# Kernel tuning notes

Measured on AMD Instinct MI355X. Metric: run time of the kernel, lower is better.

Reference implementation:

```python
import jax, jax.numpy as jnp
import numpy as np

D = 1024
H = 16
HD = D // H
N_TEXT = 256
N_VISION = 256
N_FRAMES = 12


def setup_inputs() -> dict:
    key = jax.random.key(0)
    ks = jax.random.split(key, 10)
    s = 1.0 / np.sqrt(D)
    return {
        "text_hidden_states": jax.random.normal(ks[0], (N_TEXT, D), jnp.float32),
        "vision_hidden_states": jax.random.normal(ks[1], (N_VISION, N_FRAMES, D), jnp.float32),
        "wq": jax.random.normal(ks[2], (D, D), jnp.float32) * s,
        "bq": jnp.zeros((D,), jnp.float32),
        "wk": jax.random.normal(ks[3], (D, D), jnp.float32) * s,
        "bk": jnp.zeros((D,), jnp.float32),
        "wv": jax.random.normal(ks[4], (D, D), jnp.float32) * s,
        "bv": jnp.zeros((D,), jnp.float32),
        "wo": jax.random.normal(ks[5], (D, D), jnp.float32) * s,
        "bo": jnp.zeros((D,), jnp.float32),
    }


def reference(text_hidden_states, vision_hidden_states, wq, bq, wk, bk, wv, bv, wo, bo):
    n_text = text_hidden_states.shape[0]
    n_vision, n_frames, _ = vision_hidden_states.shape
    # projections (torch Linear: x @ W.T + b)
    q = (text_hidden_states @ wq.T + bq).reshape(n_text, H, HD)            # [t,h,d]
    k = (vision_hidden_states @ wk.T + bk).reshape(n_vision, n_frames, H, HD)  # [v,f,h,d]
    v = (vision_hidden_states @ wv.T + bv).reshape(n_vision, n_frames, H, HD)  # [v,f,h,d]
    # shared query broadcast over vision batch: scores [v,h,f,t]
    scores = jnp.einsum("vfhd,thd->vhft", k, q) / jnp.sqrt(jnp.asarray(HD, scores_dtype := q.dtype))
    probs = jax.nn.softmax(scores, axis=2)  # softmax over frames (dim=2)
    # attn_output [v,t,h,d] -> [v,t,D]
    out = jnp.einsum("vfhd,vhft->vthd", v, probs).reshape(n_vision, n_text, D)
    return out @ wo.T + bo
```

## Files before the change

kernel.cpp:

```cpp
#include <hip/hip_runtime.h>

typedef short bf16x8 __attribute__((ext_vector_type(8)));
typedef float f32x4 __attribute__((ext_vector_type(4)));

__device__ __forceinline__ unsigned short f2bf(float f) {
  union { float f; unsigned u; } x; x.f = f;
  unsigned u = x.u;
  u += 0x7fffu + ((u >> 16) & 1u);
  return (unsigned short)(u >> 16);
}

__global__ __launch_bounds__(256) void cvt_all(
    const float* __restrict__ text, const float* __restrict__ vis,
    const float* __restrict__ wq, const float* __restrict__ wk,
    const float* __restrict__ wv, const float* __restrict__ wo,
    unsigned short* __restrict__ o0, unsigned short* __restrict__ o1,
    unsigned short* __restrict__ o2, unsigned short* __restrict__ o3,
    unsigned short* __restrict__ o4, unsigned short* __restrict__ o5)
{
  long i4 = (long)blockIdx.x * 256 + threadIdx.x;
  const float* src; unsigned short* dst; long base;
  if      (i4 <   65536) { src = text; dst = o0; base = 0; }
  else if (i4 <  851968) { src = vis;  dst = o1; base = 65536; }
  else if (i4 < 1114112) { src = wq;   dst = o2; base = 851968; }
  else if (i4 < 1376256) { src = wk;   dst = o3; base = 1114112; }
  else if (i4 < 1638400) { src = wv;   dst = o4; base = 1376256; }
  else                   { src = wo;   dst = o5; base = 1638400; }
  long li = i4 - base;
  float4 f = reinterpret_cast<const float4*>(src)[li];
  uint2 u;
  u.x = (unsigned)f2bf(f.x) | ((unsigned)f2bf(f.y) << 16);
  u.y = (unsigned)f2bf(f.z) | ((unsigned)f2bf(f.w) << 16);
  reinterpret_cast<uint2*>(dst)[li] = u;
}

__global__ __launch_bounds__(256) void gemm_abt_bf16(
    const unsigned short* __restrict__ A,
    const unsigned short* __restrict__ B,
    unsigned short* __restrict__ C,
    const float* __restrict__ bias,
    int K, int lda, int ldb, int ldc)
{
  __shared__ unsigned short As[64][40];
  __shared__ unsigned short Bs[64][40];
  const int m0 = blockIdx.y * 64, n0 = blockIdx.x * 64;
  const int tid = threadIdx.x;
  const int lane = tid & 63, w = tid >> 6;
  const int wm = w >> 1, wn = w & 1;
  const int r16 = lane & 15, kg = lane >> 4;
  const int srow = tid >> 2, sseg = tid & 3;

  const f32x4 fzero = {0.f, 0.f, 0.f, 0.f};
  f32x4 acc[2][2];
#pragma unroll
  for (int i = 0; i < 2; ++i)
#pragma unroll
    for (int j = 0; j < 2; ++j) acc[i][j] = fzero;

  for (int k0 = 0; k0 < K; k0 += 32) {
    __syncthreads();
    *reinterpret_cast<int4*>(&As[srow][sseg * 8]) =
        *reinterpret_cast<const int4*>(&A[(long)(m0 + srow) * lda + k0 + sseg * 8]);
    *reinterpret_cast<int4*>(&Bs[srow][sseg * 8]) =
        *reinterpret_cast<const int4*>(&B[(long)(n0 + srow) * ldb + k0 + sseg * 8]);
    __syncthreads();
    bf16x8 a[2], b[2];
#pragma unroll
    for (int i = 0; i < 2; ++i)
      a[i] = *reinterpret_cast<const bf16x8*>(&As[wm * 32 + i * 16 + r16][kg * 8]);
#pragma unroll
    for (int j = 0; j < 2; ++j)
      b[j] = *reinterpret_cast<const bf16x8*>(&Bs[wn * 32 + j * 16 + r16][kg * 8]);
#pragma unroll
    for (int i = 0; i < 2; ++i)
#pragma unroll
      for (int j = 0; j < 2; ++j)
        acc[i][j] = __builtin_amdgcn_mfma_f32_16x16x32_bf16(a[i], b[j], acc[i][j], 0, 0, 0);
  }
#pragma unroll
  for (int i = 0; i < 2; ++i) {
#pragma unroll
    for (int j = 0; j < 2; ++j) {
      const int row = m0 + wm * 32 + i * 16 + kg * 4;
      const int col = n0 + wn * 32 + j * 16 + r16;
      const float bv = bias ? bias[col] : 0.f;
#pragma unroll
      for (int r = 0; r < 4; ++r)
        C[(long)(row + r) * ldc + col] = f2bf(acc[i][j][r] + bv);
    }
  }
}

__global__ __launch_bounds__(256) void gemm_abt_bf16_kv(
    const unsigned short* __restrict__ A,
    const unsigned short* __restrict__ B0,
    const unsigned short* __restrict__ B1,
    unsigned short* __restrict__ C0,
    unsigned short* __restrict__ C1,
    const float* __restrict__ bias0,
    const float* __restrict__ bias1,
    int K, int lda, int ldb, int ldc)
{
  const unsigned short* B = blockIdx.z ? B1 : B0;
  unsigned short* C = blockIdx.z ? C1 : C0;
  const float* bias = blockIdx.z ? bias1 : bias0;

  __shared__ unsigned short As[64][40];
  __shared__ unsigned short Bs[64][40];
  const int m0 = blockIdx.y * 64, n0 = blockIdx.x * 64;
  const int tid = threadIdx.x;
  const int lane = tid & 63, w = tid >> 6;
  const int wm = w >> 1, wn = w & 1;
  const int r16 = lane & 15, kg = lane >> 4;
  const int srow = tid >> 2, sseg = tid & 3;

  const f32x4 fzero = {0.f, 0.f, 0.f, 0.f};
  f32x4 acc[2][2];
#pragma unroll
  for (int i = 0; i < 2; ++i)
#pragma unroll
    for (int j = 0; j < 2; ++j) acc[i][j] = fzero;

  for (int k0 = 0; k0 < K; k0 += 32) {
    __syncthreads();
    *reinterpret_cast<int4*>(&As[srow][sseg * 8]) =
        *reinterpret_cast<const int4*>(&A[(long)(m0 + srow) * lda + k0 + sseg * 8]);
    *reinterpret_cast<int4*>(&Bs[srow][sseg * 8]) =
        *reinterpret_cast<const int4*>(&B[(long)(n0 + srow) * ldb + k0 + sseg * 8]);
    __syncthreads();
    bf16x8 a[2], b[2];
#pragma unroll
    for (int i = 0; i < 2; ++i)
      a[i] = *reinterpret_cast<const bf16x8*>(&As[wm * 32 + i * 16 + r16][kg * 8]);
#pragma unroll
    for (int j = 0; j < 2; ++j)
      b[j] = *reinterpret_cast<const bf16x8*>(&Bs[wn * 32 + j * 16 + r16][kg * 8]);
#pragma unroll
    for (int i = 0; i < 2; ++i)
#pragma unroll
      for (int j = 0; j < 2; ++j)
        acc[i][j] = __builtin_amdgcn_mfma_f32_16x16x32_bf16(a[i], b[j], acc[i][j], 0, 0, 0);
  }
#pragma unroll
  for (int i = 0; i < 2; ++i) {
#pragma unroll
    for (int j = 0; j < 2; ++j) {
      const int row = m0 + wm * 32 + i * 16 + kg * 4;
      const int col = n0 + wn * 32 + j * 16 + r16;
      const float bv = bias ? bias[col] : 0.f;
#pragma unroll
      for (int r = 0; r < 4; ++r)
        C[(long)(row + r) * ldc + col] = f2bf(acc[i][j][r] + bv);
    }
  }
}

__global__ __launch_bounds__(256) void scores_softmax(
    const unsigned short* __restrict__ Kp,
    const unsigned short* __restrict__ Qp,
    unsigned short* __restrict__ P)
{
  const int h = blockIdx.x, v = blockIdx.y;
  const int tid = threadIdx.x, lane = tid & 63, w = tid >> 6;
  const int r16 = lane & 15, kg = lane >> 4;
  __shared__ unsigned short Ks[16][72];
  __shared__ unsigned short Qs[256][72];

  if (tid < 96) {
    const int f = tid >> 3, seg = tid & 7;
    *reinterpret_cast<int4*>(&Ks[f][seg * 8]) =
        *reinterpret_cast<const int4*>(&Kp[(long)(v * 12 + f) * 1024 + h * 64 + seg * 8]);
  } else if (tid < 128) {
    const int f = 12 + ((tid - 96) >> 3), seg = (tid - 96) & 7;
    int4 z; z.x = 0; z.y = 0; z.z = 0; z.w = 0;
    *reinterpret_cast<int4*>(&Ks[f][seg * 8]) = z;
  }
#pragma unroll
  for (int rep = 0; rep < 8; ++rep) {
    const int row = rep * 32 + (tid >> 3), seg = tid & 7;
    *reinterpret_cast<int4*>(&Qs[row][seg * 8]) =
        *reinterpret_cast<const int4*>(&Qp[(long)row * 1024 + h * 64 + seg * 8]);
  }
  __syncthreads();

  const f32x4 fzero = {0.f, 0.f, 0.f, 0.f};
  f32x4 acc[4];
#pragma unroll
  for (int j = 0; j < 4; ++j) acc[j] = fzero;

#pragma unroll
  for (int kk = 0; kk < 64; kk += 32) {
    bf16x8 a = *reinterpret_cast<const bf16x8*>(&Ks[r16][kk + kg * 8]);
#pragma unroll
    for (int j = 0; j < 4; ++j) {
      bf16x8 b = *reinterpret_cast<const bf16x8*>(&Qs[w * 64 + j * 16 + r16][kk + kg * 8]);
      acc[j] = __builtin_amdgcn_mfma_f32_16x16x32_bf16(a, b, acc[j], 0, 0, 0);
    }
  }
#pragma unroll
  for (int j = 0; j < 4; ++j) {
    float lm = -1e30f;
    if (kg < 3) {
#pragma unroll
      for (int r = 0; r < 4; ++r) lm = fmaxf(lm, acc[j][r] * 0.125f);
    }
    lm = fmaxf(lm, __shfl_xor(lm, 16));
    lm = fmaxf(lm, __shfl_xor(lm, 32));
    float p[4]; float ls = 0.f;
    if (kg < 3) {
#pragma unroll
      for (int r = 0; r < 4; ++r) { p[r] = __expf(acc[j][r] * 0.125f - lm); ls += p[r]; }
    }
    ls += __shfl_xor(ls, 16);
    ls += __shfl_xor(ls, 32);
    const float inv = 1.f / ls;
    if (kg < 3) {
      const int t = w * 64 + j * 16 + r16;
      uint2 u2;
      u2.x = (unsigned)f2bf(p[0] * inv) | ((unsigned)f2bf(p[1] * inv) << 16);
      u2.y = (unsigned)f2bf(p[2] * inv) | ((unsigned)f2bf(p[3] * inv) << 16);
      *reinterpret_cast<uint2*>(&P[((long)v * 256 + t) * 192 + h * 12 + kg * 4]) = u2;
    }
  }
}

__global__ __launch_bounds__(256) void combine(
    const unsigned short* __restrict__ VPp,
    const unsigned short* __restrict__ Wo,
    const unsigned short* __restrict__ P,
    const float* __restrict__ bo,
    float* __restrict__ out)
{
  const int wgid = blockIdx.x;
  const int xcd = wgid & 7, idx = wgid >> 3;
  const int v = ((idx & 31) << 3) | xcd;
  const int n0 = (idx >> 5) << 6;

  const int tid = threadIdx.x, lane = tid & 63, w = tid >> 6;
  const int r16 = lane & 15, kg = lane >> 4;

  __shared__ unsigned short BsAll[64 * 192];

  const unsigned short* VPv = VPp + (long)v * 12 * 1024;
#pragma unroll
  for (int hi = 0; hi < 4; ++hi) {
    const int h = (w << 2) + hi;
    const int db = h * 64;
    f32x4 accp[4] = {{0.f,0.f,0.f,0.f},{0.f,0.f,0.f,0.f},{0.f,0.f,0.f,0.f},{0.f,0.f,0.f,0.f}};
#pragma unroll
    for (int kk = 0; kk < 64; kk += 32) {
      bf16x8 a = {0,0,0,0,0,0,0,0};
      if (r16 < 12)
        a = *reinterpret_cast<const bf16x8*>(&VPv[(long)r16 * 1024 + db + kk + kg * 8]);
      bf16x8 bfr[4];
#pragma unroll
      for (int j = 0; j < 4; ++j)
        bfr[j] = *reinterpret_cast<const bf16x8*>(
            &Wo[(long)(n0 + j * 16 + r16) * 1024 + db + kk + kg * 8]);
#pragma unroll
      for (int j = 0; j < 4; ++j)
        accp[j] = __builtin_amdgcn_mfma_f32_16x16x32_bf16(a, bfr[j], accp[j], 0, 0, 0);
    }
#pragma unroll
    for (int j = 0; j < 4; ++j) {
#pragma unroll
      for (int r = 0; r < 4; ++r) {
        const int f = kg * 4 + r;
        if (f < 12) {
          const int o = j * 16 + r16;
          const int k = h * 12 + f;
          BsAll[o * 192 + (((k >> 3) ^ (o & 7)) << 3) + (k & 7)] = f2bf(accp[j][r]);
        }
      }
    }
  }

  const unsigned short* Pv = P + (long)v * 256 * 192;
  bf16x8 aP[2][4];
#pragma unroll
  for (int s = 0; s < 2; ++s)
#pragma unroll
    for (int i = 0; i < 4; ++i)
      aP[s][i] = *reinterpret_cast<const bf16x8*>(
          &Pv[(long)(w * 64 + i * 16 + r16) * 192 + s * 32 + kg * 8]);

  __syncthreads();

  f32x4 acc[4][4];
#pragma unroll
  for (int i = 0; i < 4; ++i)
#pragma unroll
    for (int j = 0; j < 4; ++j) { f32x4 z = {0.f,0.f,0.f,0.f}; acc[i][j] = z; }

#pragma unroll
  for (int s = 0; s < 6; ++s) {
    const int k0 = s * 32;
    bf16x8 b[4];
#pragma unroll
    for (int j = 0; j < 4; ++j) {
      const int row = j * 16 + r16;
      const int slot = (k0 >> 3) + kg;
      b[j] = *reinterpret_cast<const bf16x8*>(
          &BsAll[row * 192 + ((slot ^ (row & 7)) << 3)]);
    }
    bf16x8 aC[4];
#pragma unroll
    for (int i = 0; i < 4; ++i) aC[i] = aP[s & 1][i];
    if (s < 4) {
#pragma unroll
      for (int i = 0; i < 4; ++i)
        aP[s & 1][i] = *reinterpret_cast<const bf16x8*>(
            &Pv[(long)(w * 64 + i * 16 + r16) * 192 + (k0 + 64) + kg * 8]);
    }
#pragma unroll
    for (int i = 0; i < 4; ++i)
#pragma unroll
      for (int j = 0; j < 4; ++j)
        acc[i][j] = __builtin_amdgcn_mfma_f32_16x16x32_bf16(aC[i], b[j], acc[i][j], 0, 0, 0);
  }

  __syncthreads();
  float* Eps = reinterpret_cast<float*>(BsAll);
  const int c4 = lane & 15;
  const int rr = lane >> 4;
  f32x4 bias4 = *reinterpret_cast<const f32x4*>(&bo[n0 + c4 * 4]);
  const int wbase = w * 1088;

#pragma unroll
  for (int i = 0; i < 4; ++i) {
#pragma unroll
    for (int j = 0; j < 4; ++j)
#pragma unroll
      for (int r = 0; r < 4; ++r)
        Eps[wbase + (kg * 4 + r) * 68 + j * 16 + r16] = acc[i][j][r];
    asm volatile("s_waitcnt lgkmcnt(0)" ::: "memory");
#pragma unroll
    for (int q = 0; q < 4; ++q) {
      const int row16 = rr + q * 4;
      f32x4 vle = *reinterpret_cast<const f32x4*>(&Eps[wbase + row16 * 68 + c4 * 4]);
      vle += bias4;
      *reinterpret_cast<f32x4*>(
          &out[((long)v * 256 + w * 64 + i * 16 + row16) * 1024 + n0 + c4 * 4]) = vle;
    }
    asm volatile("s_waitcnt lgkmcnt(0)" ::: "memory");
  }
}

extern "C" void kernel_launch(void* const* d_in, const int* in_sizes, int n_in,
                              void* d_out, int out_size, void* d_ws, size_t ws_size,
                              hipStream_t stream) {
  const float* text = (const float*)d_in[0];
  const float* vis  = (const float*)d_in[1];
  const float* wq   = (const float*)d_in[2];
  const float* bq   = (const float*)d_in[3];
  const float* wk   = (const float*)d_in[4];
  const float* bk   = (const float*)d_in[5];
  const float* wv   = (const float*)d_in[6];
  const float* bv   = (const float*)d_in[7];
  const float* wo   = (const float*)d_in[8];
  const float* bo   = (const float*)d_in[9];
  float* out = (float*)d_out;

  unsigned short* text16 = (unsigned short*)d_ws;
  unsigned short* vis16  = text16 + 262144;
  unsigned short* wq16   = vis16  + 3145728;
  unsigned short* wk16   = wq16   + 1048576;
  unsigned short* wv16   = wk16   + 1048576;
  unsigned short* wo16   = wv16   + 1048576;
  unsigned short* q16    = wo16   + 1048576;
  unsigned short* k16    = q16    + 262144;
  unsigned short* vp16   = k16    + 3145728;
  unsigned short* P      = vp16   + 3145728;

  cvt_all<<<7424, 256, 0, stream>>>(text, vis, wq, wk, wv, wo,
                                    text16, vis16, wq16, wk16, wv16, wo16);
  gemm_abt_bf16<<<dim3(16, 4), 256, 0, stream>>>(text16, wq16, q16, bq, 1024, 1024, 1024, 1024);
  gemm_abt_bf16_kv<<<dim3(16, 48, 2), 256, 0, stream>>>(
      vis16, wk16, wv16, k16, vp16, bk, bv, 1024, 1024, 1024, 1024);
  scores_softmax<<<dim3(16, 256), 256, 0, stream>>>(k16, q16, P);
  combine<<<4096, 256, 0, stream>>>(vp16, wo16, P, bo, out);
}
```

Baseline: 232.3 us.

## Swap MFMA operand roles to write output directly without LDS transpose

The final GEMM now swaps its MFMA operands (the LDS-staged Wo-projected block becomes the A operand and P becomes B), so each lane's accumulator holds four consecutive output columns. These can be written straight to global memory as float4 with bias added, which removes the LDS epilogue staging, its barrier and its waitcnts. The bf16 stores into shared memory are also packed into 8-byte writes instead of scalar 2-byte writes. The trade-off is that each output row's stores are spread over more lanes, so coalescing may be less contiguous than in the staged path.

```diff
diff --git a/kernel.cpp b/kernel.cpp
--- a/kernel.cpp
+++ b/kernel.cpp
@@ -261,88 +261,78 @@
       for (int j = 0; j < 4; ++j)
         accp[j] = __builtin_amdgcn_mfma_f32_16x16x32_bf16(a, bfr[j], accp[j], 0, 0, 0);
     }
-#pragma unroll
-    for (int j = 0; j < 4; ++j) {
-#pragma unroll
-      for (int r = 0; r < 4; ++r) {
-        const int f = kg * 4 + r;
-        if (f < 12) {
-          const int o = j * 16 + r16;
-          const int k = h * 12 + f;
-          BsAll[o * 192 + (((k >> 3) ^ (o & 7)) << 3) + (k & 7)] = f2bf(accp[j][r]);
-        }
+    if (kg < 3) {
+      const int k = h * 12 + kg * 4;
+#pragma unroll
+      for (int j = 0; j < 4; ++j) {
+        const int o = j * 16 + r16;
+        uint2 u2;
+        u2.x = (unsigned)f2bf(accp[j][0]) | ((unsigned)f2bf(accp[j][1]) << 16);
+        u2.y = (unsigned)f2bf(accp[j][2]) | ((unsigned)f2bf(accp[j][3]) << 16);
+        *reinterpret_cast<uint2*>(
+            &BsAll[o * 192 + (((k >> 3) ^ (o & 7)) << 3) + (k & 7)]) = u2;
       }
     }
   }
 
   const unsigned short* Pv = P + (long)v * 256 * 192;
-  bf16x8 aP[2][4];
+  bf16x8 pB[2][4];
 #pragma unroll
   for (int s = 0; s < 2; ++s)
 #pragma unroll
     for (int i = 0; i < 4; ++i)
-      aP[s][i] = *reinterpret_cast<const bf16x8*>(
+      pB[s][i] = *reinterpret_cast<const bf16x8*>(
           &Pv[(long)(w * 64 + i * 16 + r16) * 192 + s * 32 + kg * 8]);
 
+  f32x4 bias4[4];
+#pragma unroll
+  for (int j = 0; j < 4; ++j)
+    bias4[j] = *reinterpret_cast<const f32x4*>(&bo[n0 + j * 16 + kg * 4]);
+
   __syncthreads();
 
   f32x4 acc[4][4];
 #pragma unroll
-  for (int i = 0; i < 4; ++i)
-#pragma unroll
-    for (int j = 0; j < 4; ++j) { f32x4 z = {0.f,0.f,0.f,0.f}; acc[i][j] = z; }
+  for (int j = 0; j < 4; ++j)
+#pragma unroll
+    for (int i = 0; i < 4; ++i) { f32x4 z = {0.f,0.f,0.f,0.f}; acc[j][i] = z; }
 
 #pragma unroll
   for (int s = 0; s < 6; ++s) {
     const int k0 = s * 32;
-    bf16x8 b[4];
+    bf16x8 zA[4];
 #pragma unroll
     for (int j = 0; j < 4; ++j) {
       const int row = j * 16 + r16;
       const int slot = (k0 >> 3) + kg;
-      b[j] = *reinterpret_cast<const bf16x8*>(
+      zA[j] = *reinterpret_cast<const bf16x8*>(
           &BsAll[row * 192 + ((slot ^ (row & 7)) << 3)]);
     }
-    bf16x8 aC[4];
-#pragma unroll
-    for (int i = 0; i < 4; ++i) aC[i] = aP[s & 1][i];
+    bf16x8 pC[4];
+#pragma unroll
+    for (int i = 0; i < 4; ++i) pC[i] = pB[s & 1][i];
     if (s < 4) {
 #pragma unroll
       for (int i = 0; i < 4; ++i)
-        aP[s & 1][i] = *reinterpret_cast<const bf16x8*>(
+        pB[s & 1][i] = *reinterpret_cast<const bf16x8*>(
             &Pv[(long)(w * 64 + i * 16 + r16) * 192 + (k0 + 64) + kg * 8]);
     }
 #pragma unroll
-    for (int i = 0; i < 4; ++i)
-#pragma unroll
-      for (int j = 0; j < 4; ++j)
-        acc[i][j] = __builtin_amdgcn_mfma_f32_16x16x32_bf16(aC[i], b[j], acc[i][j], 0, 0, 0);
-  }
-
-  __syncthreads();
-  float* Eps = reinterpret_cast<float*>(BsAll);
-  const int c4 = lane & 15;
-  const int rr = lane >> 4;
-  f32x4 bias4 = *reinterpret_cast<const f32x4*>(&bo[n0 + c4 * 4]);
-  const int wbase = w * 1088;
-
+    for (int j = 0; j < 4; ++j)
+#pragma unroll
+      for (int i = 0; i < 4; ++i)
+        acc[j][i] = __builtin_amdgcn_mfma_f32_16x16x32_bf16(zA[j], pC[i], acc[j][i], 0, 0, 0);
+  }
+
+  float* outv = out + (long)v * 256 * 1024;
 #pragma unroll
   for (int i = 0; i < 4; ++i) {
-#pragma unroll
-    for (int j = 0; j < 4; ++j)
-#pragma unroll
-      for (int r = 0; r < 4; ++r)
-        Eps[wbase + (kg * 4 + r) * 68 + j * 16 + r16] = acc[i][j][r];
-    asm volatile("s_waitcnt lgkmcnt(0)" ::: "memory");
-#pragma unroll
-    for (int q = 0; q < 4; ++q) {
-      const int row16 = rr + q * 4;
-      f32x4 vle = *reinterpret_cast<const f32x4*>(&Eps[wbase + row16 * 68 + c4 * 4]);
-      vle += bias4;
-      *reinterpret_cast<f32x4*>(
-          &out[((long)v * 256 + w * 64 + i * 16 + row16) * 1024 + n0 + c4 * 4]) = vle;
-    }
-    asm volatile("s_waitcnt lgkmcnt(0)" ::: "memory");
+    const long tbase = (long)(w * 64 + i * 16 + r16) * 1024;
+#pragma unroll
+    for (int j = 0; j < 4; ++j) {
+      f32x4 vle = acc[j][i] + bias4[j];
+      *reinterpret_cast<f32x4*>(&outv[tbase + n0 + j * 16 + kg * 4]) = vle;
+    }
   }
 }
 
```

After: 232.9 us. Within noise of the previous version (+0.3%).
